# Kernel optimization log

Measured on AMD Instinct MI355X. Metric: run time of the kernel, lower is better.

The kernel has to match this reference:

```python
import jax, jax.numpy as jnp
import numpy as np

B, T, D, H, L = 4, 2048, 256, 4, 2
HD = D // H
VOCAB, MAX_BITS, MLP_H = 32, 64, 64


def setup_inputs() -> dict:
    key = jax.random.key(0)
    ks = jax.random.split(key, 20)
    s = 0.02
    n = lambda k, shp: (jax.random.normal(k, shp, jnp.float32) * s)
    inp = {
        'tokens': jax.random.randint(ks[0], (B, T), 0, VOCAB),
        'embed': n(ks[1], (VOCAB, D)),
        'ln1_w': jnp.ones((L, D)), 'ln1_b': jnp.zeros((L, D)),
        'qkv_w': n(ks[2], (L, D, 3 * D)), 'qkv_b': jnp.zeros((L, 3 * D)),
        'proj_w': n(ks[3], (L, D, D)), 'proj_b': jnp.zeros((L, D)),
        'ln2_w': jnp.ones((L, D)), 'ln2_b': jnp.zeros((L, D)),
        'ffn1_w': n(ks[4], (L, D, 4 * D)), 'ffn1_b': jnp.zeros((L, 4 * D)),
        'ffn2_w': n(ks[5], (L, 4 * D, D)), 'ffn2_b': jnp.zeros((L, D)),
        'lnf_w': jnp.ones((D,)), 'lnf_b': jnp.zeros((D,)),
        'out_queries': n(ks[6], (MAX_BITS * 2, D)),
        'outp_w': n(ks[7], (D, 1)), 'outp_b': jnp.zeros((1,)),
        'mlp_w1': n(ks[8], (3, MLP_H)), 'mlp_b1': jnp.zeros((MLP_H,)),
        'mlp_w2': n(ks[9], (MLP_H, MLP_H)), 'mlp_b2': jnp.zeros((MLP_H,)),
        'mlp_w3': n(ks[10], (MLP_H, 2)), 'mlp_b3': jnp.zeros((2,)),
    }
    return inp


def _layernorm(x, w, b, eps=1e-5):
    mu = jnp.mean(x, axis=-1, keepdims=True)
    var = jnp.mean(jnp.square(x - mu), axis=-1, keepdims=True)
    return (x - mu) * jax.lax.rsqrt(var + eps) * w + b


def _rope_tables(t_len, hd):
    inv_freq = 1.0 / (10000.0 ** (jnp.arange(0, hd, 2, dtype=jnp.float32) / hd))
    freqs = jnp.outer(jnp.arange(t_len, dtype=jnp.float32), inv_freq)  # [T, hd/2]
    emb = jnp.concatenate([freqs, freqs], axis=-1)                     # [T, hd]
    return jnp.cos(emb)[None, :, None, :], jnp.sin(emb)[None, :, None, :]


def _rotate_half(x):
    x1, x2 = x[..., : x.shape[-1] // 2], x[..., x.shape[-1] // 2:]
    return jnp.concatenate([-x2, x1], axis=-1)


def _attention(x, qkv_w, qkv_b, proj_w, proj_b):
    b, t, c = x.shape
    qkv = (x @ qkv_w + qkv_b).reshape(b, t, 3, H, HD)
    q, k, v = qkv[:, :, 0], qkv[:, :, 1], qkv[:, :, 2]  # [B,T,H,HD]
    cos, sin = _rope_tables(t, HD)
    q = q * cos + _rotate_half(q) * sin
    k = k * cos + _rotate_half(k) * sin
    scores = jnp.einsum('bthd,bshd->bhts', q, k) / jnp.sqrt(jnp.float32(HD))
    causal = jnp.tril(jnp.ones((t, t), dtype=bool))
    scores = jnp.where(causal, scores, -jnp.inf)
    attn = jax.nn.softmax(scores, axis=-1)
    out = jnp.einsum('bhts,bshd->bthd', attn, v).reshape(b, t, c)
    return out @ proj_w + proj_b


def reference(tokens, embed, ln1_w, ln1_b, qkv_w, qkv_b, proj_w, proj_b,
              ln2_w, ln2_b, ffn1_w, ffn1_b, ffn2_w, ffn2_b, lnf_w, lnf_b,
              out_queries, outp_w, outp_b,
              mlp_w1, mlp_b1, mlp_w2, mlp_b2, mlp_w3, mlp_b3):
    x = embed[tokens]  # [B,T,D]
    for l in range(L):
        x = x + _attention(_layernorm(x, ln1_w[l], ln1_b[l]),
                           qkv_w[l], qkv_b[l], proj_w[l], proj_b[l])
        h = _layernorm(x, ln2_w[l], ln2_b[l])
        h = jax.nn.gelu(h @ ffn1_w[l] + ffn1_b[l], approximate=False)
        x = x + (h @ ffn2_w[l] + ffn2_b[l])
    x = _layernorm(x, lnf_w, lnf_b)
    # query cross-attention for bit-pair selection
    q_scores = jnp.einsum('qd,btd->bqt', out_queries, x) / jnp.sqrt(jnp.float32(D))
    q_attn = jax.nn.softmax(q_scores, axis=-1)           # [B, 2*MAX_BITS, T]
    selected = jnp.einsum('bqt,btd->bqd', q_attn, x)
    bits = jax.nn.sigmoid((selected @ outp_w + outp_b)[..., 0])
    pairs = bits.reshape(-1, MAX_BITS, 2)                # [B, MAX_BITS, 2]

    # sequential full-adder over bits
    def step(carry, ab):  # carry [B], ab [B,2]
        z = jnp.concatenate([ab, carry[:, None]], axis=-1)  # [B,3]
        h = jax.nn.relu(z @ mlp_w1 + mlp_b1)
        h = jax.nn.relu(h @ mlp_w2 + mlp_b2)
        o = jax.nn.sigmoid(h @ mlp_w3 + mlp_b3)
        return o[:, 1], o[:, 0]

    carry0 = jnp.zeros((pairs.shape[0],), jnp.float32)
    carry, sum_bits = jax.lax.scan(step, carry0, jnp.swapaxes(pairs, 0, 1))
    sum_all = jnp.concatenate([sum_bits.T, carry[:, None]], axis=1)  # [B, MAX_BITS+1]
    return sum_all, pairs, q_attn
```

## Files before the change

kernel.cpp:

```cpp
#include <hip/hip_runtime.h>
#include <hip/hip_bf16.h>

#define BB 4
#define TT 2048
#define DD 256
#define HH 4
#define HDD 64
#define NROW 8192
#define NQ 128

typedef __hip_bfloat16 bf16;
typedef __attribute__((ext_vector_type(8))) short bf8v;
typedef __attribute__((ext_vector_type(4))) short bf4v;
typedef __attribute__((ext_vector_type(4))) float f4v;
typedef __attribute__((ext_vector_type(2))) unsigned int u2v;

__device__ __forceinline__ bf16 f2b(float v){ return __float2bfloat16(v); }
__device__ __forceinline__ short f2bs(float v){
    bf16 h = __float2bfloat16(v);
    return *reinterpret_cast<short*>(&h);
}
__device__ __forceinline__ float bs2f(short s){
    bf16 h = *reinterpret_cast<bf16*>(&s);
    return __bfloat162float(h);
}
__device__ __forceinline__ float rl(float v, int l){
    return __uint_as_float(__builtin_amdgcn_readlane(__float_as_uint(v), l));
}

__device__ __forceinline__ void gll16(const void* g, void* l){
    __builtin_amdgcn_global_load_lds((const __attribute__((address_space(1))) unsigned int*)g,
                                     (__attribute__((address_space(3))) unsigned int*)l, 16, 0, 0);
}

#define DPP_ROR_ADD(v, ctrl) \
    ((v) + __int_as_float(__builtin_amdgcn_update_dpp(0, __float_as_int(v), (ctrl), 0xF, 0xF, false)))
#define DPP_ROR_MAX(v, ctrl) \
    fmaxf((v), __int_as_float(__builtin_amdgcn_update_dpp(0, __float_as_int(v), (ctrl), 0xF, 0xF, false)))

__device__ __forceinline__ void plswap16(float v, float& a, float& b){
#if __has_builtin(__builtin_amdgcn_permlane16_swap)
    u2v r = __builtin_amdgcn_permlane16_swap(__float_as_uint(v), __float_as_uint(v), false, false);
    a = __uint_as_float(r.x); b = __uint_as_float(r.y);
#else
    a = v; b = v;
    asm volatile("" : "+v"(b));
    asm("v_permlane16_swap_b32 %0, %1" : "+v"(a), "+v"(b));
#endif
}
__device__ __forceinline__ void plswap32(float v, float& a, float& b){
#if __has_builtin(__builtin_amdgcn_permlane32_swap)
    u2v r = __builtin_amdgcn_permlane32_swap(__float_as_uint(v), __float_as_uint(v), false, false);
    a = __uint_as_float(r.x); b = __uint_as_float(r.y);
#else
    a = v; b = v;
    asm volatile("" : "+v"(b));
    asm("v_permlane32_swap_b32 %0, %1" : "+v"(a), "+v"(b));
#endif
}
__device__ __forceinline__ float swap16_add(float v){ float a,b; plswap16(v,a,b); return a + b; }
__device__ __forceinline__ float swap32_add(float v){ float a,b; plswap32(v,a,b); return a + b; }
__device__ __forceinline__ float swap16_max(float v){ float a,b; plswap16(v,a,b); return fmaxf(a,b); }
__device__ __forceinline__ float swap32_max(float v){ float a,b; plswap32(v,a,b); return fmaxf(a,b); }
__device__ __forceinline__ float wsum(float v){
    v = DPP_ROR_ADD(v, 0x121); v = DPP_ROR_ADD(v, 0x122);
    v = DPP_ROR_ADD(v, 0x124); v = DPP_ROR_ADD(v, 0x128);
    v = swap16_add(v); v = swap32_add(v);
    return v;
}
__device__ __forceinline__ float wmax(float v){
    v = DPP_ROR_MAX(v, 0x121); v = DPP_ROR_MAX(v, 0x122);
    v = DPP_ROR_MAX(v, 0x124); v = DPP_ROR_MAX(v, 0x128);
    v = swap16_max(v); v = swap32_max(v);
    return v;
}

#define MFMA32(A,B,C) __builtin_amdgcn_mfma_f32_16x16x32_bf16((A),(B),(C),0,0,0)
#if __has_builtin(__builtin_amdgcn_mfma_f32_16x16x16bf16_1k)
#define MFMA16(A,B,C) __builtin_amdgcn_mfma_f32_16x16x16bf16_1k((A),(B),(C),0,0,0)
#else
__device__ __forceinline__ f4v mfma16_asm(bf4v a, bf4v b, f4v c){
    f4v d;
    asm("v_mfma_f32_16x16x16_bf16 %0, %1, %2, %3" : "=v"(d) : "v"(a), "v"(b), "v"(c));
    return d;
}
#define MFMA16(A,B,C) mfma16_asm((A),(B),(C))
#endif

__global__ __launch_bounds__(256) void k_embln(const int* __restrict__ tok,
                                               const float* __restrict__ emb,
                                               const float* __restrict__ w,
                                               const float* __restrict__ b,
                                               float* __restrict__ x,
                                               bf16* __restrict__ Y){
    int row = blockIdx.x*4 + (threadIdx.x >> 6);
    int lane = threadIdx.x & 63;
    f4v v = *(const f4v*)(emb + (long)tok[row]*DD + lane*4);
    *(f4v*)(x + (long)row*DD + lane*4) = v;
    float s  = (v[0]+v[1]) + (v[2]+v[3]);
    float s2 = (v[0]*v[0]+v[1]*v[1]) + (v[2]*v[2]+v[3]*v[3]);
    s = wsum(s); s2 = wsum(s2);
    float mu  = s * (1.0f/DD);
    float var = s2 * (1.0f/DD) - mu*mu;
    float rs  = rsqrtf(var + 1e-5f);
    f4v wv4 = *(const f4v*)(w + lane*4);
    f4v bv4 = *(const f4v*)(b + lane*4);
    bf4v o;
    #pragma unroll
    for (int i=0;i<4;i++) o[i] = f2bs((v[i]-mu)*rs*wv4[i] + bv4[i]);
    *(bf4v*)(Y + (long)row*DD + lane*4) = o;
}

__global__ __launch_bounds__(256) void k_misc(const float* __restrict__ oq, bf16* __restrict__ oqb,
                                              float* __restrict__ cosT, float* __restrict__ sinT,
                                              const float* __restrict__ w2, float* __restrict__ w2t){
    int gid = blockIdx.x*256 + threadIdx.x;
    {
        int t = gid >> 5, dd = gid & 31;
        float invf = powf(10000.0f, -(float)(2*dd)/64.0f);
        float ang = (float)t * invf;
        float sn, cs;
        sincosf(ang, &sn, &cs);
        cosT[gid] = cs; sinT[gid] = sn;
    }
    if (gid < NQ*DD) oqb[gid] = f2b(oq[gid]);
    if (gid < 4096){ int j = gid >> 6, k = gid & 63; w2t[gid] = w2[k*64 + j]; }
}

__global__ __launch_bounds__(256) void k_wtall(const float* __restrict__ qkvw,
                                               const float* __restrict__ projw,
                                               const float* __restrict__ f1w,
                                               const float* __restrict__ f2w,
                                               bf16* __restrict__ wt){
    __shared__ float t[32][33];
    int z = blockIdx.z;
    int l = z >> 2, type = z & 3;
    long L = (long)l*786432;
    int K, M; const float* src; long doff;
    if (type == 0){ K=256;  M=768;  src = qkvw + (long)l*256*768;  doff = L; }
    else if (type == 1){ K=256;  M=256;  src = projw + (long)l*256*256; doff = L + 196608; }
    else if (type == 2){ K=256;  M=1024; src = f1w  + (long)l*256*1024; doff = L + 262144; }
    else               { K=1024; M=256;  src = f2w  + (long)l*1024*256; doff = L + 524288; }
    int m0 = blockIdx.x*32, k0 = blockIdx.y*32;
    if (m0 >= M || k0 >= K) return;
    bf16* dst = wt + doff;
    int tx = threadIdx.x, ty = threadIdx.y;
    #pragma unroll
    for (int i=0;i<4;i++)
        t[ty+i*8][tx] = src[(long)(k0+ty+i*8)*M + m0 + tx];
    __syncthreads();
    #pragma unroll
    for (int i=0;i<4;i++)
        dst[(long)(m0+ty+i*8)*K + k0 + tx] = f2b(t[tx][ty+i*8]);
}

__global__ __launch_bounds__(256) void k_lnb(const float* __restrict__ X,
                                             const float* __restrict__ w,
                                             const float* __restrict__ b,
                                             bf16* __restrict__ Y){
    int row = blockIdx.x*4 + (threadIdx.x >> 6);
    int lane = threadIdx.x & 63;
    f4v v = *(const f4v*)(X + (long)row*DD + lane*4);
    float s  = (v[0]+v[1]) + (v[2]+v[3]);
    float s2 = (v[0]*v[0]+v[1]*v[1]) + (v[2]*v[2]+v[3]*v[3]);
    s = wsum(s); s2 = wsum(s2);
    float mu  = s * (1.0f/DD);
    float var = s2 * (1.0f/DD) - mu*mu;
    float rs  = rsqrtf(var + 1e-5f);
    f4v wv4 = *(const f4v*)(w + lane*4);
    f4v bv4 = *(const f4v*)(b + lane*4);
    bf4v o;
    #pragma unroll
    for (int i=0;i<4;i++) o[i] = f2bs((v[i]-mu)*rs*wv4[i] + bv4[i]);
    *(bf4v*)(Y + (long)row*DD + lane*4) = o;
}

__global__ __launch_bounds__(256) void k_lnf(const float* __restrict__ X,
                                             const float* __restrict__ w,
                                             const float* __restrict__ b,
                                             const float* __restrict__ ow,
                                             bf16* __restrict__ Yb,
                                             float* __restrict__ g){
    int row = blockIdx.x*4 + (threadIdx.x >> 6);
    int lane = threadIdx.x & 63;
    f4v v = *(const f4v*)(X + (long)row*DD + lane*4);
    float s  = (v[0]+v[1]) + (v[2]+v[3]);
    float s2 = (v[0]*v[0]+v[1]*v[1]) + (v[2]*v[2]+v[3]*v[3]);
    s = wsum(s); s2 = wsum(s2);
    float mu  = s * (1.0f/DD);
    float var = s2 * (1.0f/DD) - mu*mu;
    float rs  = rsqrtf(var + 1e-5f);
    f4v wv4 = *(const f4v*)(w + lane*4);
    f4v bv4 = *(const f4v*)(b + lane*4);
    f4v ov4 = *(const f4v*)(ow + lane*4);
    bf4v o;
    float gp = 0.f;
    #pragma unroll
    for (int i=0;i<4;i++){
        float y = (v[i]-mu)*rs*wv4[i] + bv4[i];
        o[i] = f2bs(y);
        gp += y * ov4[i];
    }
    *(bf4v*)(Yb + (long)row*DD + lane*4) = o;
    gp = wsum(gp);
    if (lane == 0) g[row] = gp;
}

__global__ __launch_bounds__(256) void k_mgemm(const bf16* __restrict__ A,
                                               const bf16* __restrict__ Wt,
                                               const float* __restrict__ bias,
                                               float* __restrict__ Cf,
                                               bf16* __restrict__ Cb,
                                               int K, int M, int mode){
    __shared__ short As[128*32];
    __shared__ short Ws[64*32];
    int tid = threadIdx.x;
    int lane = tid & 63, wv = tid >> 6;
    int n0 = blockIdx.y * 128, m0 = blockIdx.x * 64;
    int rbase = (wv >> 1) * 64, cbase = (wv & 1) * 32;
    f4v acc[4][2] = {};
    int s2 = tid + 256;
    int wvo = wv * 512;
    for (int k0 = 0; k0 < K; k0 += 32){
        __syncthreads();
        gll16(A  + (long)(n0 + (tid>>2))*K + k0 + ((tid&3)<<3), &As[wvo]);
        gll16(A  + (long)(n0 + (s2 >>2))*K + k0 + ((s2 &3)<<3), &As[2048 + wvo]);
        gll16(Wt + (long)(m0 + (tid>>2))*K + k0 + ((tid&3)<<3), &Ws[wvo]);
        __syncthreads();
        bf8v af[4], bfr[2];
        int k8 = (lane >> 4) << 3;
        #pragma unroll
        for (int i=0;i<4;i++) af[i]  = *(bf8v*)&As[(rbase + i*16 + (lane&15))*32 + k8];
        #pragma unroll
        for (int j=0;j<2;j++) bfr[j] = *(bf8v*)&Ws[(cbase + j*16 + (lane&15))*32 + k8];
        #pragma unroll
        for (int i=0;i<4;i++)
            #pragma unroll
            for (int j=0;j<2;j++)
                acc[i][j] = MFMA32(af[i], bfr[j], acc[i][j]);
    }
    int rq = (lane >> 4) * 4;
    int cl = lane & 15;
    #pragma unroll
    for (int i=0;i<4;i++){
        #pragma unroll
        for (int j=0;j<2;j++){
            int m = m0 + cbase + j*16 + cl;
            float bs = bias[m];
            #pragma unroll
            for (int r=0;r<4;r++){
                int n = n0 + rbase + i*16 + rq + r;
                float v = acc[i][j][r] + bs;
                long idx = (long)n*M + m;
                if (mode == 0)      Cf[idx] = v;
                else if (mode == 1) Cf[idx] += v;
                else if (mode == 2) Cb[idx] = f2b(0.5f*v*(1.0f + erff(v*0.70710678118654752f)));
                else                Cb[idx] = f2b(v);
            }
        }
    }
}

__global__ __launch_bounds__(256) void k_mgemmQKV(const bf16* __restrict__ A,
                                                  const bf16* __restrict__ Wt,
                                                  const float* __restrict__ bias,
                                                  const float* __restrict__ cosT,
                                                  const float* __restrict__ sinT,
                                                  bf16* __restrict__ qb,
                                                  bf16* __restrict__ kb,
                                                  bf16* __restrict__ vt){
    __shared__ short As[128*32];
    __shared__ short Ws[64*32];
    __shared__ short E[128][68];
    const int K = 256, M = 768;
    int tid = threadIdx.x;
    int lane = tid & 63, wv = tid >> 6;
    int n0 = blockIdx.y * 128, m0 = blockIdx.x * 64;
    int rbase = (wv >> 1) * 64, cbase = (wv & 1) * 32;
    f4v acc[4][2] = {};
    int s2 = tid + 256;
    int wvo = wv * 512;
    for (int k0 = 0; k0 < K; k0 += 32){
        __syncthreads();
        gll16(A  + (long)(n0 + (tid>>2))*K + k0 + ((tid&3)<<3), &As[wvo]);
        gll16(A  + (long)(n0 + (s2 >>2))*K + k0 + ((s2 &3)<<3), &As[2048 + wvo]);
        gll16(Wt + (long)(m0 + (tid>>2))*K + k0 + ((tid&3)<<3), &Ws[wvo]);
        __syncthreads();
        bf8v af[4], bfr[2];
        int k8 = (lane >> 4) << 3;
        #pragma unroll
        for (int i=0;i<4;i++) af[i]  = *(bf8v*)&As[(rbase + i*16 + (lane&15))*32 + k8];
        #pragma unroll
        for (int j=0;j<2;j++) bfr[j] = *(bf8v*)&Ws[(cbase + j*16 + (lane&15))*32 + k8];
        #pragma unroll
        for (int i=0;i<4;i++)
            #pragma unroll
            for (int j=0;j<2;j++)
                acc[i][j] = MFMA32(af[i], bfr[j], acc[i][j]);
    }
    int rq = (lane >> 4) * 4;
    int cl = lane & 15;
    #pragma unroll
    for (int i=0;i<4;i++){
        #pragma unroll
        for (int j=0;j<2;j++){
            int cc = cbase + j*16 + cl;
            float bs = bias[m0 + cc];
            #pragma unroll
            for (int r=0;r<4;r++)
                E[rbase + i*16 + rq + r][cc] = f2bs(acc[i][j][r] + bs);
        }
    }
    __syncthreads();
    int part = m0 >> 8;
    int h = (m0 >> 6) & 3;
    int b = n0 >> 11;
    int t0 = n0 & 2047;
    int bh = b*HH + h;
    if (part < 2){
        bf16* dst0 = part ? kb : qb;
        int r2 = tid >> 2;
        int c0 = (tid & 3) * 16;
        int cpx = c0 ^ 32;
        #pragma unroll
        for (int half=0; half<2; half++){
            int row = half*64 + r2;
            int t = t0 + row;
            bf8v e0 = *(bf8v*)&E[row][c0];
            bf8v e1 = *(bf8v*)&E[row][c0+8];
            bf8v p0 = *(bf8v*)&E[row][cpx];
            bf8v p1 = *(bf8v*)&E[row][cpx+8];
            const float* ct = cosT + t*32;
            const float* st = sinT + t*32;
            short o[16];
            #pragma unroll
            for (int i=0;i<8;i++){
                int d = c0 + i, dd = d & 31;
                float cs = ct[dd], sn = st[dd];
                float v = bs2f(e0[i]), v2 = bs2f(p0[i]);
                o[i] = f2bs((d < 32) ? (v*cs - v2*sn) : (v*cs + v2*sn));
            }
            #pragma unroll
            for (int i=0;i<8;i++){
                int d = c0 + 8 + i, dd = d & 31;
                float cs = ct[dd], sn = st[dd];
                float v = bs2f(e1[i]), v2 = bs2f(p1[i]);
                o[8+i] = f2bs((d < 32) ? (v*cs - v2*sn) : (v*cs + v2*sn));
            }
            short* dp = (short*)dst0 + ((long)bh*TT + t)*64 + c0;
            *(bf8v*)dp     = *(bf8v*)&o[0];
            *(bf8v*)(dp+8) = *(bf8v*)&o[8];
        }
    } else {
        int tIdx0 = t0 >> 6;
        int d  = (tid & 127) >> 1;
        int k0 = (tid & 1) * 32;
        int tt = tid >> 7;
        short o[32];
        #pragma unroll
        for (int k=0;k<32;k++) o[k] = E[tt*64 + k0 + k][d];
        short* dp = (short*)vt + (((long)bh*32 + tIdx0 + tt)*64 + d)*64 + k0;
        *(bf8v*)dp      = *(bf8v*)&o[0];
        *(bf8v*)(dp+8)  = *(bf8v*)&o[8];
        *(bf8v*)(dp+16) = *(bf8v*)&o[16];
        *(bf8v*)(dp+24) = *(bf8v*)&o[24];
    }
}

__global__ __launch_bounds__(256) void k_fattn(const bf16* __restrict__ qb,
                                               const bf16* __restrict__ kb,
                                               const bf16* __restrict__ vt,
                                               bf16* __restrict__ ob){
    __shared__ short Ks[2][128][72];
    __shared__ short Vs[2][128][68];
    int bh = blockIdx.y;
    int qt = (int)(gridDim.x - 1) - (int)blockIdx.x;
    int tid = threadIdx.x;
    int lane = tid & 63, w = tid >> 6;
    int col = lane & 15, quad = lane >> 4;
    int q0 = qt*64 + w*16;
    const bf16* qp = qb + ((long)bh*TT + q0 + col)*64 + quad*8;
    bf8v bq0 = *(const bf8v*)(qp);
    bf8v bq1 = *(const bf8v*)(qp + 32);
    f4v oc[4] = {};
    float lsum = 0.f;
    int qglob = q0 + col;
    int ktmax = qt >> 1;
    int srow = tid >> 1, sc0 = (tid & 1) * 32;
    const short* kgb = (const short*)kb + ((long)bh*TT + srow)*64 + sc0;
    const short* vgb = (const short*)vt + (((long)bh*32)*64 + srow)*64 + sc0;

    bf8v pk0 = *(const bf8v*)(kgb);
    bf8v pk1 = *(const bf8v*)(kgb + 8);
    bf8v pk2 = *(const bf8v*)(kgb + 16);
    bf8v pk3 = *(const bf8v*)(kgb + 24);
    bf8v pv0 = *(const bf8v*)(vgb);
    bf8v pv1 = *(const bf8v*)(vgb + 8);
    bf8v pv2 = *(const bf8v*)(vgb + 16);
    bf8v pv3 = *(const bf8v*)(vgb + 24);
    *(bf8v*)&Ks[0][srow][sc0]      = pk0;
    *(bf8v*)&Ks[0][srow][sc0 + 8]  = pk1;
    *(bf8v*)&Ks[0][srow][sc0 + 16] = pk2;
    *(bf8v*)&Ks[0][srow][sc0 + 24] = pk3;
    *(bf8v*)&Vs[0][srow][sc0]      = pv0;
    *(bf8v*)&Vs[0][srow][sc0 + 8]  = pv1;
    *(bf8v*)&Vs[0][srow][sc0 + 16] = pv2;
    *(bf8v*)&Vs[0][srow][sc0 + 24] = pv3;

    int buf = 0;
    for (int kt=0; kt<=ktmax; kt++){
        __syncthreads();
        bool more = (kt < ktmax);
        if (more){
            const short* kg = kgb + (long)(kt+1)*8192;
            const short* vg = vgb + (long)(kt+1)*8192;
            pk0 = *(const bf8v*)(kg);      pk1 = *(const bf8v*)(kg + 8);
            pk2 = *(const bf8v*)(kg + 16); pk3 = *(const bf8v*)(kg + 24);
            pv0 = *(const bf8v*)(vg);      pv1 = *(const bf8v*)(vg + 8);
            pv2 = *(const bf8v*)(vg + 16); pv3 = *(const bf8v*)(vg + 24);
        }
        bool diag = (kt == ktmax);
        int ntmax = diag ? ((qt & 1) ? 4 + w : w) : 7;
        bf4v bp[8];
        #pragma unroll
        for (int nt=0; nt<8; nt++){
            if (nt > ntmax) continue;
            bf8v ka0 = *(const bf8v*)&Ks[buf][nt*16 + col][quad*8];
            bf8v ka1 = *(const bf8v*)&Ks[buf][nt*16 + col][32 + quad*8];
            f4v st = {};
            st = MFMA32(ka0, bq0, st);
            st = MFMA32(ka1, bq1, st);
            int key0 = kt*128 + nt*16 + quad*4;
            bf4v pb;
            #pragma unroll
            for (int r=0; r<4; r++){
                float e = __expf(st[r]*0.125f);
                if (diag && (key0 + r > qglob)) e = 0.f;
                lsum += e;
                pb[r] = f2bs(e);
            }
            bp[nt] = pb;
        }
        #pragma unroll
        for (int dt=0; dt<4; dt++){
            #pragma unroll
            for (int nt=0; nt<8; nt++){
                if (nt > ntmax) continue;
                bf4v va = *(const bf4v*)&Vs[buf][(nt>>2)*64 + dt*16 + col][(nt&3)*16 + quad*4];
                oc[dt] = MFMA16(va, bp[nt], oc[dt]);
            }
        }
        if (more){
            *(bf8v*)&Ks[buf^1][srow][sc0]      = pk0;
            *(bf8v*)&Ks[buf^1][srow][sc0 + 8]  = pk1;
            *(bf8v*)&Ks[buf^1][srow][sc0 + 16] = pk2;
            *(bf8v*)&Ks[buf^1][srow][sc0 + 24] = pk3;
            *(bf8v*)&Vs[buf^1][srow][sc0]      = pv0;
            *(bf8v*)&Vs[buf^1][srow][sc0 + 8]  = pv1;
            *(bf8v*)&Vs[buf^1][srow][sc0 + 16] = pv2;
            *(bf8v*)&Vs[buf^1][srow][sc0 + 24] = pv3;
        }
        buf ^= 1;
    }
    lsum += __shfl_xor(lsum, 16, 64);
    lsum += __shfl_xor(lsum, 32, 64);
    float linv = 1.0f / lsum;

    int b = bh / HH, h = bh % HH;
    long obase = ((long)b*TT + q0 + col)*DD + h*64 + quad*4;
    #pragma unroll
    for (int dt=0; dt<4; dt++){
        bf4v o4;
        #pragma unroll
        for (int r=0; r<4; r++) o4[r] = f2bs(oc[dt][r]*linv);
        *(bf4v*)(ob + obase + dt*16) = o4;
    }
}

__global__ __launch_bounds__(256) void k_score(const bf16* __restrict__ oqb,
                                               const bf16* __restrict__ xfb,
                                               float* __restrict__ S){
    int b = blockIdx.y, t0 = blockIdx.x*64;
    int tid = threadIdx.x, lane = tid & 63, w = tid >> 6;
    int col = lane & 15, quad = lane >> 4, k8 = quad << 3;
    const bf16* xb = xfb + (long)b*TT*DD;
    f4v acc[2][4] = {};
    #pragma unroll
    for (int ko=0; ko<8; ko++){
        int kk = ko*32 + k8;
        bf8v a0 = *(const bf8v*)(oqb + (long)(w*32 +      col)*DD + kk);
        bf8v a1 = *(const bf8v*)(oqb + (long)(w*32 + 16 + col)*DD + kk);
        #pragma unroll
        for (int bt=0; bt<4; bt++){
            bf8v bv = *(const bf8v*)(xb + (long)(t0 + bt*16 + col)*DD + kk);
            acc[0][bt] = MFMA32(a0, bv, acc[0][bt]);
            acc[1][bt] = MFMA32(a1, bv, acc[1][bt]);
        }
    }
    #pragma unroll
    for (int qt2=0; qt2<2; qt2++){
        #pragma unroll
        for (int bt=0; bt<4; bt++){
            #pragma unroll
            for (int r=0; r<4; r++){
                int q = w*32 + qt2*16 + quad*4 + r;
                S[((long)b*NQ + q)*TT + t0 + bt*16 + col] = acc[qt2][bt][r]*0.0625f;
            }
        }
    }
}

__global__ __launch_bounds__(256) void k_psoft(const float* __restrict__ S,
                                               const float* __restrict__ g,
                                               const float* __restrict__ obias,
                                               float* __restrict__ out_qattn,
                                               float* __restrict__ out_pairs,
                                               float* __restrict__ bits){
    __shared__ float cmax[4], cs[4], cg[4];
    int bq = blockIdx.x, b = bq >> 7;
    int tid = threadIdx.x, wv = tid >> 6, lane = tid & 63;
    const f4v* S4 = (const f4v*)(S + (long)bq*TT);
    f4v s0 = S4[tid], s1 = S4[tid + 256];
    float lmax = fmaxf(fmaxf(fmaxf(s0[0],s0[1]), fmaxf(s0[2],s0[3])),
                       fmaxf(fmaxf(s1[0],s1[1]), fmaxf(s1[2],s1[3])));
    lmax = wmax(lmax);
    if (lane == 0) cmax[wv] = lmax;
    __syncthreads();
    float m = fmaxf(fmaxf(cmax[0],cmax[1]), fmaxf(cmax[2],cmax[3]));
    const f4v* g4 = (const f4v*)(g + (long)b*TT);
    f4v gv0 = g4[tid], gv1 = g4[tid + 256];
    f4v e0, e1;
    #pragma unroll
    for (int i=0;i<4;i++){ e0[i] = __expf(s0[i]-m); e1[i] = __expf(s1[i]-m); }
    float lsum = (e0[0]+e0[1]+e0[2]+e0[3]) + (e1[0]+e1[1]+e1[2]+e1[3]);
    float gdot = (e0[0]*gv0[0]+e0[1]*gv0[1]+e0[2]*gv0[2]+e0[3]*gv0[3])
               + (e1[0]*gv1[0]+e1[1]*gv1[1]+e1[2]*gv1[2]+e1[3]*gv1[3]);
    lsum = wsum(lsum); gdot = wsum(gdot);
    if (lane == 0){ cs[wv] = lsum; cg[wv] = gdot; }
    __syncthreads();
    float Lr = (cs[0]+cs[1]) + (cs[2]+cs[3]);
    float G  = (cg[0]+cg[1]) + (cg[2]+cg[3]);
    float inv = 1.0f / Lr;
    f4v* out4 = (f4v*)(out_qattn + (long)bq*TT);
    out4[tid]       = e0 * inv;
    out4[tid + 256] = e1 * inv;
    if (tid == 0){
        float bit = 1.0f/(1.0f + expf(-(G*inv + obias[0])));
        bits[bq] = bit;
        out_pairs[bq] = bit;
    }
}

__global__ __launch_bounds__(64) void k_scan(const float* __restrict__ bits,
                                             const float* __restrict__ w1, const float* __restrict__ b1,
                                             const float* __restrict__ w2t, const float* __restrict__ b2,
                                             const float* __restrict__ w3, const float* __restrict__ b3,
                                             float* __restrict__ out_sum){
    __shared__ __align__(16) float h1s[2][64];
    int b = blockIdx.x, lane = threadIdx.x;
    float w1c0 = w1[lane], w1c1 = w1[64 + lane], w1c2 = w1[128 + lane];
    float b1v = b1[lane], b2v = b2[lane];
    float w3c0 = w3[lane*2 + 0], w3c1 = w3[lane*2 + 1];
    float b30 = b3[0], b31 = b3[1];
    const f4v* wrow = (const f4v*)(w2t + (long)lane*64);
    f4v c0v = wrow[0],  c1v = wrow[1],  c2v = wrow[2],  c3v = wrow[3],
        c4v = wrow[4],  c5v = wrow[5],  c6v = wrow[6],  c7v = wrow[7],
        c8v = wrow[8],  c9v = wrow[9],  cav = wrow[10], cbv = wrow[11],
        ccv = wrow[12], cdv = wrow[13], cev = wrow[14], cfv = wrow[15];
    float z0v = bits[b*128 + lane*2 + 0];
    float z1v = bits[b*128 + lane*2 + 1];
    float carry = 0.f;
    for (int step=0; step<64; step++){
        float z0 = rl(z0v, step);
        float z1 = rl(z1v, step);
        float h1 = fmaxf(z0*w1c0 + z1*w1c1 + carry*w1c2 + b1v, 0.f);
        float* hb = h1s[step & 1];
        hb[lane] = h1;
        __syncthreads();
        const f4v* hv = (const f4v*)hb;
        f4v va = hv[0]*c0v,  vb = hv[1]*c1v,  vc = hv[2]*c2v,   vd = hv[3]*c3v;
        va += hv[4]*c4v;   vb += hv[5]*c5v;   vc += hv[6]*c6v;   vd += hv[7]*c7v;
        va += hv[8]*c8v;   vb += hv[9]*c9v;   vc += hv[10]*cav;  vd += hv[11]*cbv;
        va += hv[12]*ccv;  vb += hv[13]*cdv;  vc += hv[14]*cev;  vd += hv[15]*cfv;
        f4v vs = (va + vb) + (vc + vd);
        float h2 = fmaxf(((vs[0] + vs[1]) + (vs[2] + vs[3])) + b2v, 0.f);
        float t0 = h2*w3c0, t1 = h2*w3c1;
        t0 = DPP_ROR_ADD(t0, 0x121); t1 = DPP_ROR_ADD(t1, 0x121);
        t0 = DPP_ROR_ADD(t0, 0x122); t1 = DPP_ROR_ADD(t1, 0x122);
        t0 = DPP_ROR_ADD(t0, 0x124); t1 = DPP_ROR_ADD(t1, 0x124);
        t0 = DPP_ROR_ADD(t0, 0x128); t1 = DPP_ROR_ADD(t1, 0x128);
        t0 = swap16_add(t0); t1 = swap16_add(t1);
        t0 = swap32_add(t0); t1 = swap32_add(t1);
        float o0 = 1.0f/(1.0f + __expf(-(t0 + b30)));
        carry    = 1.0f/(1.0f + __expf(-(t1 + b31)));
        if (lane == 0) out_sum[b*65 + step] = o0;
    }
    if (lane == 0) out_sum[b*65 + 64] = carry;
}

extern "C" void kernel_launch(void* const* d_in, const int* in_sizes, int n_in,
                              void* d_out, int out_size, void* d_ws, size_t ws_size,
                              hipStream_t stream){
    const int*   tok   = (const int*)d_in[0];
    const float* emb   = (const float*)d_in[1];
    const float* ln1w  = (const float*)d_in[2];
    const float* ln1b  = (const float*)d_in[3];
    const float* qkvw  = (const float*)d_in[4];
    const float* qkvb  = (const float*)d_in[5];
    const float* projw = (const float*)d_in[6];
    const float* projb = (const float*)d_in[7];
    const float* ln2w  = (const float*)d_in[8];
    const float* ln2b  = (const float*)d_in[9];
    const float* f1w   = (const float*)d_in[10];
    const float* f1b   = (const float*)d_in[11];
    const float* f2w   = (const float*)d_in[12];
    const float* f2bb  = (const float*)d_in[13];
    const float* lnfw  = (const float*)d_in[14];
    const float* lnfb  = (const float*)d_in[15];
    const float* oq    = (const float*)d_in[16];
    const float* ow    = (const float*)d_in[17];
    const float* obias = (const float*)d_in[18];
    const float* w1    = (const float*)d_in[19];
    const float* b1    = (const float*)d_in[20];
    const float* w2    = (const float*)d_in[21];
    const float* b2    = (const float*)d_in[22];
    const float* w3    = (const float*)d_in[23];
    const float* b3    = (const float*)d_in[24];
    float* out = (float*)d_out;

    const long MB = 1048576;
    char* W = (char*)d_ws;
    float* x     = (float*)(W);
    bf16*  attnb = (bf16*)(W + 8*MB);
    bf16*  hb    = (bf16*)(W + 16*MB);
    bf16*  qb    = (bf16*)(W + 32*MB);
    bf16*  kb    = (bf16*)(W + 36*MB);
    bf16*  vt    = (bf16*)(W + 44*MB);
    bf16*  xnb   = (bf16*)(W + 48*MB);
    bf16*  wt    = (bf16*)(W + 52*MB);
    float* bits  = (float*)(W + 55*MB);
    bf16*  oqb   = (bf16*)(W + 56*MB);
    float* cosT  = (float*)(W + 57*MB);
    float* sinT  = cosT + 65536;
    float* w2t   = (float*)(W + 58*MB);
    bf16*  xfb   = (bf16*)(W + 32*MB);
    float* g     = (float*)(W + 36*MB);
    float* S     = (float*)(W + 40*MB);

    k_wtall<<<dim3(32, 32, 8), dim3(32,8), 0, stream>>>(qkvw, projw, f1w, f2w, wt);
    k_misc<<<256, 256, 0, stream>>>(oq, oqb, cosT, sinT, w2, w2t);

    k_embln<<<NROW/4, 256, 0, stream>>>(tok, emb, ln1w, ln1b, x, xnb);
    for (int l=0; l<2; l++){
        long L = (long)l*786432;
        if (l) k_lnb<<<NROW/4, 256, 0, stream>>>(x, ln1w + l*DD, ln1b + l*DD, xnb);
        k_mgemmQKV<<<dim3(768/64, 64), 256, 0, stream>>>(
            xnb, wt + L, qkvb + l*768, cosT, sinT, qb, kb, vt);
        k_fattn<<<dim3(TT/64, BB*HH), 256, 0, stream>>>(qb, kb, vt, attnb);
        k_mgemm<<<dim3(256/64, 64), 256, 0, stream>>>(
            attnb, wt + L + 196608, projb + l*DD, x, (bf16*)0, 256, 256, 1);
        k_lnb<<<NROW/4, 256, 0, stream>>>(x, ln2w + l*DD, ln2b + l*DD, xnb);
        k_mgemm<<<dim3(1024/64, 64), 256, 0, stream>>>(
            xnb, wt + L + 262144, f1b + l*1024, (float*)0, hb, 256, 1024, 2);
        k_mgemm<<<dim3(256/64, 64), 256, 0, stream>>>(
            hb, wt + L + 524288, f2bb + l*DD, x, (bf16*)0, 1024, 256, 1);
    }
    k_lnf<<<NROW/4, 256, 0, stream>>>(x, lnfw, lnfb, ow, xfb, g);
    k_score<<<dim3(TT/64, BB), 256, 0, stream>>>(oqb, xfb, S);
    k_psoft<<<BB*NQ, 256, 0, stream>>>(S, g, obias, out + 772, out + 260, bits);
    k_scan<<<4, 64, 0, stream>>>(bits, w1, b1, w2t, b2, w3, b3, out);
}
```

Baseline: 400.7 us.

## Process two 64-query tiles per attention block to reuse staged K/V

The flash-attention kernel now assigns 128 query rows per block, split into two 64-row halves that share each K/V tile loaded into shared memory. This halves K/V staging loads and barrier cycles per query. The grid shrinks to half as many blocks, which lowers parallelism and worsens causal load imbalance, and it doubles accumulator register usage, which may reduce occupancy.

```diff
diff --git a/kernel.cpp b/kernel.cpp
--- a/kernel.cpp
+++ b/kernel.cpp
@@ -378,14 +378,19 @@
     int tid = threadIdx.x;
     int lane = tid & 63, w = tid >> 6;
     int col = lane & 15, quad = lane >> 4;
-    int q0 = qt*64 + w*16;
-    const bf16* qp = qb + ((long)bh*TT + q0 + col)*64 + quad*8;
-    bf8v bq0 = *(const bf8v*)(qp);
-    bf8v bq1 = *(const bf8v*)(qp + 32);
-    f4v oc[4] = {};
-    float lsum = 0.f;
-    int qglob = q0 + col;
-    int ktmax = qt >> 1;
+    int q0A = qt*128 + w*16;
+    int q0B = q0A + 64;
+    const bf16* qpA = qb + ((long)bh*TT + q0A + col)*64 + quad*8;
+    const bf16* qpB = qb + ((long)bh*TT + q0B + col)*64 + quad*8;
+    bf8v bqA0 = *(const bf8v*)(qpA);
+    bf8v bqA1 = *(const bf8v*)(qpA + 32);
+    bf8v bqB0 = *(const bf8v*)(qpB);
+    bf8v bqB1 = *(const bf8v*)(qpB + 32);
+    f4v ocA[4] = {}, ocB[4] = {};
+    float lsumA = 0.f, lsumB = 0.f;
+    int qglobA = q0A + col;
+    int qglobB = q0B + col;
+    int ktmax = qt;
     int srow = tid >> 1, sc0 = (tid & 1) * 32;
     const short* kgb = (const short*)kb + ((long)bh*TT + srow)*64 + sc0;
     const short* vgb = (const short*)vt + (((long)bh*32)*64 + srow)*64 + sc0;
@@ -420,34 +425,52 @@
             pv2 = *(const bf8v*)(vg + 16); pv3 = *(const bf8v*)(vg + 24);
         }
         bool diag = (kt == ktmax);
-        int ntmax = diag ? ((qt & 1) ? 4 + w : w) : 7;
-        bf4v bp[8];
+        int ntA = diag ? w : 7;
+        int ntB = diag ? 4 + w : 7;
+        bf4v bpA[8], bpB[8];
         #pragma unroll
         for (int nt=0; nt<8; nt++){
-            if (nt > ntmax) continue;
+            if (nt > ntB) continue;
             bf8v ka0 = *(const bf8v*)&Ks[buf][nt*16 + col][quad*8];
             bf8v ka1 = *(const bf8v*)&Ks[buf][nt*16 + col][32 + quad*8];
-            f4v st = {};
-            st = MFMA32(ka0, bq0, st);
-            st = MFMA32(ka1, bq1, st);
             int key0 = kt*128 + nt*16 + quad*4;
-            bf4v pb;
-            #pragma unroll
-            for (int r=0; r<4; r++){
-                float e = __expf(st[r]*0.125f);
-                if (diag && (key0 + r > qglob)) e = 0.f;
-                lsum += e;
-                pb[r] = f2bs(e);
+            if (nt <= ntA){
+                f4v st = {};
+                st = MFMA32(ka0, bqA0, st);
+                st = MFMA32(ka1, bqA1, st);
+                bf4v pb;
+                #pragma unroll
+                for (int r=0; r<4; r++){
+                    float e = __expf(st[r]*0.125f);
+                    if (diag && (key0 + r > qglobA)) e = 0.f;
+                    lsumA += e;
+                    pb[r] = f2bs(e);
+                }
+                bpA[nt] = pb;
             }
-            bp[nt] = pb;
+            {
+                f4v st = {};
+                st = MFMA32(ka0, bqB0, st);
+                st = MFMA32(ka1, bqB1, st);
+                bf4v pb;
+                #pragma unroll
+                for (int r=0; r<4; r++){
+                    float e = __expf(st[r]*0.125f);
+                    if (diag && (key0 + r > qglobB)) e = 0.f;
+                    lsumB += e;
+                    pb[r] = f2bs(e);
+                }
+                bpB[nt] = pb;
+            }
         }
         #pragma unroll
         for (int dt=0; dt<4; dt++){
             #pragma unroll
             for (int nt=0; nt<8; nt++){
-                if (nt > ntmax) continue;
+                if (nt > ntB) continue;
                 bf4v va = *(const bf4v*)&Vs[buf][(nt>>2)*64 + dt*16 + col][(nt&3)*16 + quad*4];
-                oc[dt] = MFMA16(va, bp[nt], oc[dt]);
+                if (nt <= ntA) ocA[dt] = MFMA16(va, bpA[nt], ocA[dt]);
+                ocB[dt] = MFMA16(va, bpB[nt], ocB[dt]);
             }
         }
         if (more){
@@ -462,18 +485,26 @@
         }
         buf ^= 1;
     }
-    lsum += __shfl_xor(lsum, 16, 64);
-    lsum += __shfl_xor(lsum, 32, 64);
-    float linv = 1.0f / lsum;
+    lsumA += __shfl_xor(lsumA, 16, 64);
+    lsumA += __shfl_xor(lsumA, 32, 64);
+    lsumB += __shfl_xor(lsumB, 16, 64);
+    lsumB += __shfl_xor(lsumB, 32, 64);
+    float linvA = 1.0f / lsumA;
+    float linvB = 1.0f / lsumB;
 
     int b = bh / HH, h = bh % HH;
-    long obase = ((long)b*TT + q0 + col)*DD + h*64 + quad*4;
+    long obaseA = ((long)b*TT + q0A + col)*DD + h*64 + quad*4;
+    long obaseB = ((long)b*TT + q0B + col)*DD + h*64 + quad*4;
     #pragma unroll
     for (int dt=0; dt<4; dt++){
-        bf4v o4;
-        #pragma unroll
-        for (int r=0; r<4; r++) o4[r] = f2bs(oc[dt][r]*linv);
-        *(bf4v*)(ob + obase + dt*16) = o4;
+        bf4v o4A, o4B;
+        #pragma unroll
+        for (int r=0; r<4; r++){
+            o4A[r] = f2bs(ocA[dt][r]*linvA);
+            o4B[r] = f2bs(ocB[dt][r]*linvB);
+        }
+        *(bf4v*)(ob + obaseA + dt*16) = o4A;
+        *(bf4v*)(ob + obaseB + dt*16) = o4B;
     }
 }
 
@@ -656,7 +687,7 @@
         if (l) k_lnb<<<NROW/4, 256, 0, stream>>>(x, ln1w + l*DD, ln1b + l*DD, xnb);
         k_mgemmQKV<<<dim3(768/64, 64), 256, 0, stream>>>(
             xnb, wt + L, qkvb + l*768, cosT, sinT, qb, kb, vt);
-        k_fattn<<<dim3(TT/64, BB*HH), 256, 0, stream>>>(qb, kb, vt, attnb);
+        k_fattn<<<dim3(TT/128, BB*HH), 256, 0, stream>>>(qb, kb, vt, attnb);
         k_mgemm<<<dim3(256/64, 64), 256, 0, stream>>>(
             attnb, wt + L + 196608, projb + l*DD, x, (bf16*)0, 256, 256, 1);
         k_lnb<<<NROW/4, 256, 0, stream>>>(x, ln2w + l*DD, ln2b + l*DD, xnb);
```

New measurement: 413.3 us. 1.03x slower.
